# Kernel optimization log

Hardware: AMD Instinct MI355X
Metric: run time of the kernel (lower is better)

Reference implementation:

```python
import jax, jax.numpy as jnp
import numpy as np

DIM = 1024
HEADS = 16
DIM_HEAD = 64
INNER = HEADS * DIM_HEAD  # 1024
SCALE = DIM_HEAD ** -0.5


def setup_inputs() -> dict:
    key = jax.random.key(0)
    ks = jax.random.split(key, 5)
    b, n = 4, 2048
    x = jax.random.normal(ks[0], (b, n, DIM), dtype=jnp.float32)
    # nn.Linear weights, stored as (in, out) for x @ W
    w_q = jax.random.normal(ks[1], (DIM, INNER), dtype=jnp.float32) / np.sqrt(DIM)
    w_kv = jax.random.normal(ks[2], (DIM, 2 * DIM_HEAD), dtype=jnp.float32) / np.sqrt(DIM)
    w_out = jax.random.normal(ks[3], (INNER, DIM), dtype=jnp.float32) / np.sqrt(INNER)
    b_out = jax.random.normal(ks[4], (DIM,), dtype=jnp.float32) * 0.01
    return {"x": x, "w_q": w_q, "w_kv": w_kv, "w_out": w_out, "b_out": b_out}


def reference(x, w_q, w_kv, w_out, b_out):
    b, n, _ = x.shape
    # Q: [b, h, n, d]; K/V: single shared head [b, n, d]
    q = (x @ w_q).reshape(b, n, HEADS, DIM_HEAD).transpose(0, 2, 1, 3)
    kv = x @ w_kv  # [b, n, 2d]
    k, v = kv[..., :DIM_HEAD], kv[..., DIM_HEAD:]
    # scores: broadcast shared K across heads
    dots = jnp.einsum('bhnd,bmd->bhnm', q, k) * SCALE  # [b,h,n,n]
    attn = jax.nn.softmax(dots, axis=-1)
    out = jnp.einsum('bhnm,bmd->bhnd', attn, v)  # shared V across heads
    out = out.transpose(0, 2, 1, 3).reshape(b, n, INNER)
    return out @ w_out + b_out
```

## Files before the change

### kernel.cpp

```cpp
#include <hip/hip_runtime.h>
#include <hip/hip_bf16.h>
#include <stdint.h>

#define SEQ    2048
#define NBATCH 4
#define NHEADS 16
#define DHEAD  64
#define MODELD 1024
#define QKVN   1152
#define MROWS  (NBATCH*SEQ)
#define SCALE_LOG2E 0.1803368801111244f

typedef __bf16 bf16x8 __attribute__((ext_vector_type(8)));
typedef float  f32x4  __attribute__((ext_vector_type(4)));

typedef __attribute__((address_space(1))) void* as1_void_p;
typedef __attribute__((address_space(3))) void* as3_void_p;

__device__ __forceinline__ void gld_lds16(const void* g, void* l) {
  __builtin_amdgcn_global_load_lds((as1_void_p)(g), (as3_void_p)(l), 16, 0, 0);
}

__device__ __forceinline__ ushort f2bf(float f) {
  union { float f; uint32_t i; } t; t.f = f;
  uint32_t r = (t.i + 0x7fffu + ((t.i >> 16) & 1u)) >> 16;
  return (ushort)r;
}
__device__ __forceinline__ uint32_t pack_bf16(float a, float b) {
  union { __hip_bfloat162 h2; uint32_t u; } cv;
  cv.h2 = __float22bfloat162_rn(make_float2(a, b));
  return cv.u;
}

__global__ __launch_bounds__(256)
void f32_to_bf16(const float* __restrict__ src, ushort* __restrict__ dst) {
  const int i = (blockIdx.x * 256 + threadIdx.x) * 4;
  const float4 v = *(const float4*)(src + i);
  ushort4 o;
  o.x = f2bf(v.x); o.y = f2bf(v.y); o.z = f2bf(v.z); o.w = f2bf(v.w);
  *(ushort4*)(dst + i) = o;
}

__global__ __launch_bounds__(256)
void transpose_f32_bf16(const float* __restrict__ src, ushort* __restrict__ dst,
                        int R, int C, float scale) {
  __shared__ float tile[32][33];
  const int tx = threadIdx.x & 31, ty = threadIdx.x >> 5;
  const int c0 = blockIdx.x * 32, r0 = blockIdx.y * 32;
#pragma unroll
  for (int j = 0; j < 4; j++)
    tile[ty*4 + j][tx] = src[(size_t)(r0 + ty*4 + j) * C + c0 + tx];
  __syncthreads();
#pragma unroll
  for (int j = 0; j < 4; j++)
    dst[(size_t)(c0 + ty*4 + j) * R + r0 + tx] = f2bf(tile[tx][ty*4 + j] * scale);
}

template <bool OUT_F32>
__global__ __launch_bounds__(256)
void gemm_bt(const ushort* __restrict__ A, const ushort* __restrict__ Bt,
             void* __restrict__ Cp, const float* __restrict__ bias,
             ushort* __restrict__ VT,
             int K, int lda, int ldb, int ldc) {
  __shared__ __attribute__((aligned(16))) ushort As[128*32];
  __shared__ __attribute__((aligned(16))) ushort Bs[128*32];
  const int tid = threadIdx.x;
  const int w = tid >> 6, lane = tid & 63;
  const int quad = lane >> 4, m16 = lane & 15;
  const int bm0 = blockIdx.y * 128, bn0 = blockIdx.x * 128;
  f32x4 acc[4][4] = {};

  const int ar0 = w*32 + (lane >> 2);
  const int ac0 = (lane & 3) * 8;
  const ushort* Ag = A  + (size_t)(bm0 + ar0) * lda + ac0;
  const ushort* Bg = Bt + (size_t)(bn0 + ar0) * ldb + ac0;
  ushort* AsW = As + (w*32)*32;
  ushort* BsW = Bs + (w*32)*32;
  const int wm = (w >> 1) * 64, wn = (w & 1) * 64;

  for (int kb = 0; kb < K; kb += 32) {
    gld_lds16(Ag + kb,                   AsW);
    gld_lds16(Ag + (size_t)16*lda + kb,  AsW + 16*32);
    gld_lds16(Bg + kb,                   BsW);
    gld_lds16(Bg + (size_t)16*ldb + kb,  BsW + 16*32);
    __syncthreads();
    bf16x8 af[4], bfr[4];
#pragma unroll
    for (int mi = 0; mi < 4; mi++)
      af[mi] = *(const bf16x8*)(As + (wm + mi*16 + m16)*32 + quad*8);
#pragma unroll
    for (int ni = 0; ni < 4; ni++)
      bfr[ni] = *(const bf16x8*)(Bs + (wn + ni*16 + m16)*32 + quad*8);
#pragma unroll
    for (int mi = 0; mi < 4; mi++)
#pragma unroll
      for (int ni = 0; ni < 4; ni++)
        acc[mi][ni] = __builtin_amdgcn_mfma_f32_16x16x32_bf16(
            af[mi], bfr[ni], acc[mi][ni], 0, 0, 0);
    __syncthreads();
  }

#pragma unroll
  for (int ni = 0; ni < 4; ni++) {
    const int col = bn0 + wn + ni*16 + m16;
    const float bv = bias ? bias[col] : 0.0f;
#pragma unroll
    for (int mi = 0; mi < 4; mi++) {
#pragma unroll
      for (int r = 0; r < 4; r++) {
        const int row = bm0 + wm + mi*16 + quad*4 + r;
        const float v = acc[mi][ni][r] + bv;
        if (OUT_F32) ((float*)Cp)[(size_t)row*ldc + col] = v;
        else         ((ushort*)Cp)[(size_t)row*ldc + col] = f2bf(v);
        if (VT && col >= 1088) {
          const int d = col - 1088, bb = row >> 11, n = row & 2047;
          VT[((size_t)bb * DHEAD + d) * SEQ + n] = f2bf(v);
        }
      }
    }
  }
}

__global__ __launch_bounds__(256, 2)
void mqa_attn(const ushort* __restrict__ qkv, const ushort* __restrict__ vT,
              ushort* __restrict__ attn_out) {
  __shared__ __attribute__((aligned(16))) ushort Ks[64*72];
  __shared__ __attribute__((aligned(16))) ushort Vs[64*72];
  __shared__ __attribute__((aligned(16))) ushort pbuf[4][64*40];

  const int tid = threadIdx.x;
  const int w = tid >> 6, lane = tid & 63;
  const int quad = lane >> 4, m16 = lane & 15;
  const int h = blockIdx.y, b = blockIdx.z;
  const size_t rowbase = (size_t)b * SEQ;
  const int q0 = blockIdx.x * 256 + w * 64;
  const ushort* vTb = vT + (size_t)b * DHEAD * SEQ;
  ushort* pb = pbuf[w];

  const int srow = tid >> 3, scol = (tid & 7) * 8;
  const ushort* kgbase = qkv + (rowbase + srow) * QKVN + 1024 + scol;
  const ushort* vgbase = vTb + (size_t)srow * SEQ + scol;

  bf16x8 qf[4][2];
#pragma unroll
  for (int qt = 0; qt < 4; qt++) {
    const ushort* qrow = qkv + (rowbase + q0 + qt*16 + m16) * QKVN + h * DHEAD;
    qf[qt][0] = *(const bf16x8*)(qrow + quad*8);
    qf[qt][1] = *(const bf16x8*)(qrow + 32 + quad*8);
  }

  f32x4 o[4][4] = {};
  float l_loc[4] = {};

  uint4 kreg0 = *(const uint4*)(kgbase);
  uint4 kreg1 = *(const uint4*)(kgbase + (size_t)32 * QKVN);
  uint4 vreg0 = *(const uint4*)(vgbase);
  uint4 vreg1 = *(const uint4*)(vgbase + 32 * SEQ);

  for (int kv0 = 0; kv0 < SEQ; kv0 += 64) {
    __syncthreads();
    *(uint4*)(Ks + (srow     )*72 + scol) = kreg0;
    *(uint4*)(Ks + (srow + 32)*72 + scol) = kreg1;
    *(uint4*)(Vs + (srow     )*72 + scol) = vreg0;
    *(uint4*)(Vs + (srow + 32)*72 + scol) = vreg1;
    __syncthreads();

    const int kvn = (kv0 + 64) & (SEQ - 1);
    kreg0 = *(const uint4*)(kgbase + (size_t)(kvn     ) * QKVN);
    kreg1 = *(const uint4*)(kgbase + (size_t)(kvn + 32) * QKVN);
    vreg0 = *(const uint4*)(vgbase + kvn);
    vreg1 = *(const uint4*)(vgbase + 32 * SEQ + kvn);

#pragma unroll
    for (int kh = 0; kh < 2; kh++) {
#pragma unroll
      for (int t2 = 0; t2 < 2; t2++) {
        const int t = kh*2 + t2;
        const bf16x8 kf0 = *(const bf16x8*)(Ks + (t*16 + m16)*72 + quad*8);
        const bf16x8 kf1 = *(const bf16x8*)(Ks + (t*16 + m16)*72 + 32 + quad*8);
#pragma unroll
        for (int qt = 0; qt < 4; qt++) {
          f32x4 s = {};
          s = __builtin_amdgcn_mfma_f32_16x16x32_bf16(kf0, qf[qt][0], s, 0, 0, 0);
          s = __builtin_amdgcn_mfma_f32_16x16x32_bf16(kf1, qf[qt][1], s, 0, 0, 0);
          float p[4];
#pragma unroll
          for (int r = 0; r < 4; r++) {
            p[r] = __builtin_amdgcn_exp2f(s[r]);
            l_loc[qt] += p[r];
          }
          *(uint2*)(pb + (qt*16 + m16)*40 + t2*16 + quad*4) =
              make_uint2(pack_bf16(p[0], p[1]), pack_bf16(p[2], p[3]));
        }
      }
      asm volatile("s_waitcnt lgkmcnt(0)" ::: "memory");

      bf16x8 pf[4], vf[4];
#pragma unroll
      for (int qt = 0; qt < 4; qt++)
        pf[qt] = *(const bf16x8*)(pb + (qt*16 + m16)*40 + quad*8);
#pragma unroll
      for (int dt = 0; dt < 4; dt++)
        vf[dt] = *(const bf16x8*)(Vs + (dt*16 + m16)*72 + kh*32 + quad*8);
#pragma unroll
      for (int qt = 0; qt < 4; qt++)
#pragma unroll
        for (int dt = 0; dt < 4; dt++)
          o[qt][dt] = __builtin_amdgcn_mfma_f32_16x16x32_bf16(vf[dt], pf[qt], o[qt][dt], 0, 0, 0);
    }
  }

#pragma unroll
  for (int qt = 0; qt < 4; qt++) {
    float l = l_loc[qt];
    l += __shfl_xor(l, 16, 64);
    l += __shfl_xor(l, 32, 64);
    const float inv = 1.0f / l;
    const size_t row = rowbase + q0 + qt*16 + m16;
#pragma unroll
    for (int dt = 0; dt < 4; dt++) {
      ushort4 st;
      st.x = f2bf(o[qt][dt][0] * inv);
      st.y = f2bf(o[qt][dt][1] * inv);
      st.z = f2bf(o[qt][dt][2] * inv);
      st.w = f2bf(o[qt][dt][3] * inv);
      *(ushort4*)(attn_out + row*MODELD + h*DHEAD + dt*16 + quad*4) = st;
    }
  }
}

extern "C" void kernel_launch(void* const* d_in, const int* in_sizes, int n_in,
                              void* d_out, int out_size, void* d_ws, size_t ws_size,
                              hipStream_t stream) {
  const float* x     = (const float*)d_in[0];
  const float* w_q   = (const float*)d_in[1];
  const float* w_kv  = (const float*)d_in[2];
  const float* w_out = (const float*)d_in[3];
  const float* b_out = (const float*)d_in[4];

  ushort* wqkvT = (ushort*)d_ws;
  ushort* woutT = wqkvT + (size_t)QKVN * MODELD;
  ushort* xb    = woutT + (size_t)MODELD * MODELD;
  ushort* qkv   = xb    + (size_t)MROWS * MODELD;
  ushort* attn  = qkv   + (size_t)MROWS * QKVN;
  ushort* vTb   = attn  + (size_t)MROWS * MODELD;

  f32_to_bf16<<<(MROWS * MODELD) / 1024, 256, 0, stream>>>(x, xb);

  transpose_f32_bf16<<<dim3(MODELD/32, MODELD/32), 256, 0, stream>>>(w_q,  wqkvT, MODELD, MODELD, SCALE_LOG2E);
  transpose_f32_bf16<<<dim3(128/32,    MODELD/32), 256, 0, stream>>>(w_kv, wqkvT + (size_t)MODELD * MODELD, MODELD, 128, 1.0f);
  transpose_f32_bf16<<<dim3(MODELD/32, MODELD/32), 256, 0, stream>>>(w_out, woutT, MODELD, MODELD, 1.0f);

  gemm_bt<false><<<dim3(QKVN/128, MROWS/128), 256, 0, stream>>>(
      xb, wqkvT, (void*)qkv, nullptr, vTb, MODELD, MODELD, MODELD, QKVN);

  mqa_attn<<<dim3(SEQ/256, NHEADS, NBATCH), 256, 0, stream>>>(qkv, vTb, attn);

  gemm_bt<true><<<dim3(MODELD/128, MROWS/128), 256, 0, stream>>>(
      attn, woutT, d_out, b_out, nullptr, MODELD, MODELD, MODELD, MODELD);
}
```

Baseline: 268.2 us.

## Fuse prep kernels, halve attention query tile, skip V-transpose check per block

Merges the x conversion and three weight transposes into one launch dispatched by block index, which removes launch overhead. The attention kernel now handles 32 query rows per wave instead of 64. That doubles the grid from 512 to 1024 blocks for better CU fill and cuts register and LDS use, at the cost of reloading each K/V tile twice as often. The QKV GEMM epilogue also tests a block-uniform flag before writing the transposed V.

```diff
diff --git a/kernel.cpp b/kernel.cpp
--- a/kernel.cpp
+++ b/kernel.cpp
@@ -32,21 +32,13 @@
   return cv.u;
 }
 
-__global__ __launch_bounds__(256)
-void f32_to_bf16(const float* __restrict__ src, ushort* __restrict__ dst) {
-  const int i = (blockIdx.x * 256 + threadIdx.x) * 4;
-  const float4 v = *(const float4*)(src + i);
-  ushort4 o;
-  o.x = f2bf(v.x); o.y = f2bf(v.y); o.z = f2bf(v.z); o.w = f2bf(v.w);
-  *(ushort4*)(dst + i) = o;
-}
-
-__global__ __launch_bounds__(256)
-void transpose_f32_bf16(const float* __restrict__ src, ushort* __restrict__ dst,
-                        int R, int C, float scale) {
+__device__ __forceinline__ void do_transpose(const float* __restrict__ src,
+                                             ushort* __restrict__ dst,
+                                             int R, int C, float scale,
+                                             int gx, int gy, int tid) {
   __shared__ float tile[32][33];
-  const int tx = threadIdx.x & 31, ty = threadIdx.x >> 5;
-  const int c0 = blockIdx.x * 32, r0 = blockIdx.y * 32;
+  const int tx = tid & 31, ty = tid >> 5;
+  const int c0 = gx * 32, r0 = gy * 32;
 #pragma unroll
   for (int j = 0; j < 4; j++)
     tile[ty*4 + j][tx] = src[(size_t)(r0 + ty*4 + j) * C + c0 + tx];
@@ -54,6 +46,31 @@
 #pragma unroll
   for (int j = 0; j < 4; j++)
     dst[(size_t)(c0 + ty*4 + j) * R + r0 + tx] = f2bf(tile[tx][ty*4 + j] * scale);
+}
+
+__global__ __launch_bounds__(256)
+void prep(const float* __restrict__ x, const float* __restrict__ w_q,
+          const float* __restrict__ w_kv, const float* __restrict__ w_out,
+          ushort* __restrict__ xb, ushort* __restrict__ wqkvT,
+          ushort* __restrict__ woutT) {
+  const int bid = blockIdx.x, tid = threadIdx.x;
+  if (bid < 8192) {
+    const size_t i = ((size_t)bid * 256 + tid) * 4;
+    const float4 v = *(const float4*)(x + i);
+    ushort4 o;
+    o.x = f2bf(v.x); o.y = f2bf(v.y); o.z = f2bf(v.z); o.w = f2bf(v.w);
+    *(ushort4*)(xb + i) = o;
+  } else if (bid < 9216) {
+    const int t = bid - 8192;
+    do_transpose(w_q, wqkvT, MODELD, MODELD, SCALE_LOG2E, t & 31, t >> 5, tid);
+  } else if (bid < 9344) {
+    const int t = bid - 9216;
+    do_transpose(w_kv, wqkvT + (size_t)MODELD * MODELD, MODELD, 128, 1.0f,
+                 t & 3, t >> 2, tid);
+  } else {
+    const int t = bid - 9344;
+    do_transpose(w_out, woutT, MODELD, MODELD, 1.0f, t & 31, t >> 5, tid);
+  }
 }
 
 template <bool OUT_F32>
@@ -100,6 +117,7 @@
     __syncthreads();
   }
 
+  const bool blockHasV = (VT != nullptr) && (bn0 + 128 > 1088);
 #pragma unroll
   for (int ni = 0; ni < 4; ni++) {
     const int col = bn0 + wn + ni*16 + m16;
@@ -112,7 +130,7 @@
         const float v = acc[mi][ni][r] + bv;
         if (OUT_F32) ((float*)Cp)[(size_t)row*ldc + col] = v;
         else         ((ushort*)Cp)[(size_t)row*ldc + col] = f2bf(v);
-        if (VT && col >= 1088) {
+        if (blockHasV && col >= 1088) {
           const int d = col - 1088, bb = row >> 11, n = row & 2047;
           VT[((size_t)bb * DHEAD + d) * SEQ + n] = f2bf(v);
         }
@@ -126,14 +144,14 @@
               ushort* __restrict__ attn_out) {
   __shared__ __attribute__((aligned(16))) ushort Ks[64*72];
   __shared__ __attribute__((aligned(16))) ushort Vs[64*72];
-  __shared__ __attribute__((aligned(16))) ushort pbuf[4][64*40];
+  __shared__ __attribute__((aligned(16))) ushort pbuf[4][32*40];
 
   const int tid = threadIdx.x;
   const int w = tid >> 6, lane = tid & 63;
   const int quad = lane >> 4, m16 = lane & 15;
   const int h = blockIdx.y, b = blockIdx.z;
   const size_t rowbase = (size_t)b * SEQ;
-  const int q0 = blockIdx.x * 256 + w * 64;
+  const int q0 = blockIdx.x * 128 + w * 32;
   const ushort* vTb = vT + (size_t)b * DHEAD * SEQ;
   ushort* pb = pbuf[w];
 
@@ -141,16 +159,16 @@
   const ushort* kgbase = qkv + (rowbase + srow) * QKVN + 1024 + scol;
   const ushort* vgbase = vTb + (size_t)srow * SEQ + scol;
 
-  bf16x8 qf[4][2];
-#pragma unroll
-  for (int qt = 0; qt < 4; qt++) {
+  bf16x8 qf[2][2];
+#pragma unroll
+  for (int qt = 0; qt < 2; qt++) {
     const ushort* qrow = qkv + (rowbase + q0 + qt*16 + m16) * QKVN + h * DHEAD;
     qf[qt][0] = *(const bf16x8*)(qrow + quad*8);
     qf[qt][1] = *(const bf16x8*)(qrow + 32 + quad*8);
   }
 
-  f32x4 o[4][4] = {};
-  float l_loc[4] = {};
+  f32x4 o[2][4] = {};
+  float l_loc[2] = {};
 
   uint4 kreg0 = *(const uint4*)(kgbase);
   uint4 kreg1 = *(const uint4*)(kgbase + (size_t)32 * QKVN);
@@ -179,7 +197,7 @@
         const bf16x8 kf0 = *(const bf16x8*)(Ks + (t*16 + m16)*72 + quad*8);
         const bf16x8 kf1 = *(const bf16x8*)(Ks + (t*16 + m16)*72 + 32 + quad*8);
 #pragma unroll
-        for (int qt = 0; qt < 4; qt++) {
+        for (int qt = 0; qt < 2; qt++) {
           f32x4 s = {};
           s = __builtin_amdgcn_mfma_f32_16x16x32_bf16(kf0, qf[qt][0], s, 0, 0, 0);
           s = __builtin_amdgcn_mfma_f32_16x16x32_bf16(kf1, qf[qt][1], s, 0, 0, 0);
@@ -195,15 +213,15 @@
       }
       asm volatile("s_waitcnt lgkmcnt(0)" ::: "memory");
 
-      bf16x8 pf[4], vf[4];
-#pragma unroll
-      for (int qt = 0; qt < 4; qt++)
+      bf16x8 pf[2], vf[4];
+#pragma unroll
+      for (int qt = 0; qt < 2; qt++)
         pf[qt] = *(const bf16x8*)(pb + (qt*16 + m16)*40 + quad*8);
 #pragma unroll
       for (int dt = 0; dt < 4; dt++)
         vf[dt] = *(const bf16x8*)(Vs + (dt*16 + m16)*72 + kh*32 + quad*8);
 #pragma unroll
-      for (int qt = 0; qt < 4; qt++)
+      for (int qt = 0; qt < 2; qt++)
 #pragma unroll
         for (int dt = 0; dt < 4; dt++)
           o[qt][dt] = __builtin_amdgcn_mfma_f32_16x16x32_bf16(vf[dt], pf[qt], o[qt][dt], 0, 0, 0);
@@ -211,7 +229,7 @@
   }
 
 #pragma unroll
-  for (int qt = 0; qt < 4; qt++) {
+  for (int qt = 0; qt < 2; qt++) {
     float l = l_loc[qt];
     l += __shfl_xor(l, 16, 64);
     l += __shfl_xor(l, 32, 64);
@@ -245,16 +263,12 @@
   ushort* attn  = qkv   + (size_t)MROWS * QKVN;
   ushort* vTb   = attn  + (size_t)MROWS * MODELD;
 
-  f32_to_bf16<<<(MROWS * MODELD) / 1024, 256, 0, stream>>>(x, xb);
-
-  transpose_f32_bf16<<<dim3(MODELD/32, MODELD/32), 256, 0, stream>>>(w_q,  wqkvT, MODELD, MODELD, SCALE_LOG2E);
-  transpose_f32_bf16<<<dim3(128/32,    MODELD/32), 256, 0, stream>>>(w_kv, wqkvT + (size_t)MODELD * MODELD, MODELD, 128, 1.0f);
-  transpose_f32_bf16<<<dim3(MODELD/32, MODELD/32), 256, 0, stream>>>(w_out, woutT, MODELD, MODELD, 1.0f);
+  prep<<<10368, 256, 0, stream>>>(x, w_q, w_kv, w_out, xb, wqkvT, woutT);
 
   gemm_bt<false><<<dim3(QKVN/128, MROWS/128), 256, 0, stream>>>(
       xb, wqkvT, (void*)qkv, nullptr, vTb, MODELD, MODELD, MODELD, QKVN);
 
-  mqa_attn<<<dim3(SEQ/256, NHEADS, NBATCH), 256, 0, stream>>>(qkv, vTb, attn);
+  mqa_attn<<<dim3(SEQ/128, NHEADS, NBATCH), 256, 0, stream>>>(qkv, vTb, attn);
 
   gemm_bt<true><<<dim3(MODELD/128, MROWS/128), 256, 0, stream>>>(
       attn, woutT, d_out, b_out, nullptr, MODELD, MODELD, MODELD, MODELD);
```

After: 262.7 us. 1.02x faster.
